# Optimization experiments

Measured on AMD Instinct MI355X. Metric: run time of the kernel, lower is better.

The kernel has to match this reference:

```python
import jax, jax.numpy as jnp
import numpy as np

N = 50000      # nodes
E = 800000     # edges
IN = 128       # in_channels
H = 64         # hidden (= edge_dim)
OUT = 64       # out_channels
BN_EPS = 1e-5


def _bn(h, gamma, beta):
    # BatchNorm1d in training mode: per-feature batch statistics
    mu = h.mean(axis=0)
    var = h.var(axis=0)
    return gamma * (h - mu) * jax.lax.rsqrt(var + BN_EPS) + beta


def _gine_layer(x, src, dst, edge_attr, We, be, W1, b1, g, bb, W2, b2):
    # edge_attr projected to node feature dim: [E, d_in]
    ea = edge_attr @ We.T + be
    # message: relu(x_j + lin(edge_attr)); x_j = x[src]
    m = jax.nn.relu(x[src] + ea)
    # scatter-add aggregate at destination nodes
    agg = jax.ops.segment_sum(m, dst, num_segments=x.shape[0])
    # (1 + eps) * x_r with eps = 0
    out = agg + x
    # MLP: Linear -> BN -> ReLU -> Linear
    h = jax.nn.relu(_bn(out @ W1.T + b1, g, bb))
    return h @ W2.T + b2


def setup_inputs() -> dict:
    key = jax.random.key(0)
    ks = jax.random.split(key, 12)

    def glorot(k, shape):
        return jax.random.normal(k, shape, jnp.float32) / np.float32(np.sqrt(shape[1]))

    return {
        "x": jax.random.normal(ks[0], (N, IN), jnp.float32),
        "edge_index": jax.random.randint(ks[1], (2, E), 0, N, jnp.int64),
        "edge_attr": jax.random.normal(ks[2], (E, H), jnp.float32),
        # layer 0
        "We0": glorot(ks[3], (IN, H)), "be0": jnp.zeros((IN,), jnp.float32),
        "W1_0": glorot(ks[4], (H, IN)), "b1_0": jnp.zeros((H,), jnp.float32),
        "g0": jnp.ones((H,), jnp.float32), "bb0": jnp.zeros((H,), jnp.float32),
        "W2_0": glorot(ks[5], (H, H)), "b2_0": jnp.zeros((H,), jnp.float32),
        # layer 1
        "We1": glorot(ks[6], (H, H)), "be1": jnp.zeros((H,), jnp.float32),
        "W1_1": glorot(ks[7], (H, H)), "b1_1": jnp.zeros((H,), jnp.float32),
        "g1": jnp.ones((H,), jnp.float32), "bb1": jnp.zeros((H,), jnp.float32),
        "W2_1": glorot(ks[8], (OUT, H)), "b2_1": jnp.zeros((OUT,), jnp.float32),
    }


def reference(x, edge_index, edge_attr,
              We0, be0, W1_0, b1_0, g0, bb0, W2_0, b2_0,
              We1, be1, W1_1, b1_1, g1, bb1, W2_1, b2_1):
    src, dst = edge_index[0], edge_index[1]
    h = _gine_layer(x, src, dst, edge_attr, We0, be0, W1_0, b1_0, g0, bb0, W2_0, b2_0)
    h = jax.nn.relu(h)  # dropout p=0.0 -> identity
    return _gine_layer(h, src, dst, edge_attr, We1, be1, W1_1, b1_1, g1, bb1, W2_1, b2_1)
```

## Files before the change

kernel.cpp:

```cpp
#include <hip/hip_runtime.h>
#include <hip/hip_bf16.h>


typedef short short8 __attribute__((ext_vector_type(8)));
typedef float f32x4 __attribute__((ext_vector_type(4)));

__device__ __forceinline__ short f2bf(float x) {
    unsigned u = __float_as_uint(x);
    unsigned r = (u + 0x7fffu + ((u >> 16) & 1u)) >> 16;
    return (short)r;
}
__device__ __forceinline__ float bf2f(unsigned short u) {
    return __uint_as_float(((unsigned)u) << 16);
}

__global__ __launch_bounds__(256) void hist_kernel(
    const int* __restrict__ ei, int* __restrict__ cnt, int E)
{
    int e = blockIdx.x * 256 + threadIdx.x;
    if (e < E) atomicAdd(&cnt[ei[E + e]], 1);
}

__global__ __launch_bounds__(1024) void scan_kernel(
    const int* __restrict__ cnt, int* __restrict__ offs,
    int* __restrict__ cursor, int N)
{
    __shared__ int wsum[16];
    __shared__ int chunk_base;
    int tid = threadIdx.x;
    int lane = tid & 63, wid = tid >> 6;
    if (tid == 0) chunk_base = 0;
    __syncthreads();
    for (int start = 0; start < N; start += 1024) {
        int i = start + tid;
        int v = (i < N) ? cnt[i] : 0;
        int s = v;
#pragma unroll
        for (int d = 1; d < 64; d <<= 1) {
            int t = __shfl_up(s, d);
            if (lane >= d) s += t;
        }
        if (lane == 63) wsum[wid] = s;
        __syncthreads();
        int wbase = 0;
        for (int w = 0; w < wid; ++w) wbase += wsum[w];
        int excl = chunk_base + wbase + s - v;
        if (i < N) { offs[i] = excl; cursor[i] = excl; }
        int tot = 0;
        for (int w = 0; w < 16; ++w) tot += wsum[w];
        __syncthreads();
        if (tid == 0) chunk_base += tot;
        __syncthreads();
    }
    if (threadIdx.x == 0) offs[N] = chunk_base;
}

__global__ __launch_bounds__(256) void scatter_kernel(
    const int* __restrict__ ei, int* __restrict__ cursor,
    int* __restrict__ inv, int E)
{
    int e = blockIdx.x * 256 + threadIdx.x;
    if (e >= E) return;
    int d = ei[E + e];
    int pos = atomicAdd(&cursor[d], 1);
    inv[e] = pos;
}

__global__ __launch_bounds__(256) void xcast_kernel(
    const float* __restrict__ x, unsigned short* __restrict__ xb, int total)
{
    for (int i = blockIdx.x * 256 + threadIdx.x; i < total; i += gridDim.x * 256)
        xb[i] = (unsigned short)f2bf(x[i]);
}

template<int DIN>
__global__ __launch_bounds__(256) void edge2_kernel(
    const unsigned short* __restrict__ xb,
    const int*    __restrict__ ei,
    const float*  __restrict__ eattr,
    const short*  __restrict__ WeB,
    const float*  __restrict__ be,
    const short*  __restrict__ W1B,
    const int*    __restrict__ inv,
    unsigned short* __restrict__ pbuf,
    int E)
{
    constexpr int S = DIN + 8;
    constexpr int KK = DIN / 32;
    __shared__ short lds[4][16][S];
    const int wave = threadIdx.x >> 6;
    const int lane = threadIdx.x & 63;
    const int ebase = (blockIdx.x * 4 + wave) * 16;
    if (ebase >= E) return;
    const int g = lane >> 4, c = lane & 15;
    short* myl = &lds[wave][0][0];

    int ce = ebase + c; if (ce >= E) ce = E - 1;
    int se_c = ei[ce];

    int sp[4];
#pragma unroll
    for (int r = 0; r < 4; ++r) {
        int e = ebase + g * 4 + r;
        sp[r] = (e < E) ? inv[e] : -1;
    }

    const float* ar = eattr + (size_t)ce * 64 + g * 8;
    f32x4 a0 = *(const f32x4*)(ar);
    f32x4 a1 = *(const f32x4*)(ar + 4);
    f32x4 a2v = *(const f32x4*)(ar + 32);
    f32x4 a3 = *(const f32x4*)(ar + 36);

    short8 xv[KK];
    const unsigned short* xr = xb + (size_t)se_c * DIN + g * 8;
#pragma unroll
    for (int kk = 0; kk < KK; ++kk)
        xv[kk] = *(const short8*)(xr + kk * 32);
    __builtin_amdgcn_sched_barrier(0);

    short8 afr0, afr1;
    afr0[0]=f2bf(a0[0]); afr0[1]=f2bf(a0[1]); afr0[2]=f2bf(a0[2]); afr0[3]=f2bf(a0[3]);
    afr0[4]=f2bf(a1[0]); afr0[5]=f2bf(a1[1]); afr0[6]=f2bf(a1[2]); afr0[7]=f2bf(a1[3]);
    afr1[0]=f2bf(a2v[0]); afr1[1]=f2bf(a2v[1]); afr1[2]=f2bf(a2v[2]); afr1[3]=f2bf(a2v[3]);
    afr1[4]=f2bf(a3[0]); afr1[5]=f2bf(a3[1]); afr1[6]=f2bf(a3[2]); afr1[7]=f2bf(a3[3]);

#pragma unroll
    for (int fc = 0; fc < DIN / 16; ++fc) {
        const short* brow = WeB + (size_t)(fc * 16 + c) * 64 + g * 8;
        short8 b0 = *(const short8*)(brow);
        short8 b1 = *(const short8*)(brow + 32);
        f32x4 acc = {0.f, 0.f, 0.f, 0.f};
        acc = __builtin_amdgcn_mfma_f32_16x16x32_bf16(afr0, b0, acc, 0, 0, 0);
        acc = __builtin_amdgcn_mfma_f32_16x16x32_bf16(afr1, b1, acc, 0, 0, 0);
        const int f = fc * 16 + c;
        const float bev = be[f];
#pragma unroll
        for (int r = 0; r < 4; ++r)
            myl[(g * 4 + r) * S + f] = f2bf(acc[r] + bev);
    }

    asm volatile("s_waitcnt lgkmcnt(0)" ::: "memory");
    __builtin_amdgcn_sched_barrier(0);

    short8 a2[KK];
#pragma unroll
    for (int kk = 0; kk < KK; ++kk) {
        short8 v = *(const short8*)(myl + c * S + kk * 32 + g * 8);
#pragma unroll
        for (int j = 0; j < 8; ++j) {
            float f = bf2f((unsigned short)v[j]) + bf2f((unsigned short)xv[kk][j]);
            a2[kk][j] = f2bf(fmaxf(f, 0.f));
        }
    }

#pragma unroll
    for (int cc = 0; cc < 4; ++cc) {
        f32x4 acc2 = {0.f, 0.f, 0.f, 0.f};
#pragma unroll
        for (int kk = 0; kk < KK; ++kk) {
            short8 b0 = *(const short8*)(W1B + (size_t)(cc * 16 + c) * DIN + kk * 32 + g * 8);
            acc2 = __builtin_amdgcn_mfma_f32_16x16x32_bf16(a2[kk], b0, acc2, 0, 0, 0);
        }
#pragma unroll
        for (int r = 0; r < 4; ++r)
            if (sp[r] >= 0)
                pbuf[(size_t)sp[r] * 64 + cc * 16 + c] = (unsigned short)f2bf(acc2[r]);
    }
}

__global__ __launch_bounds__(256) void edge1_kernel(
    const unsigned short* __restrict__ yb,
    const int*    __restrict__ ei,
    const float*  __restrict__ eattr,
    const short*  __restrict__ WeB,
    const float*  __restrict__ be,
    const int*    __restrict__ inv,
    unsigned short* __restrict__ pbuf,
    int E)
{
    constexpr int S = 72;
    __shared__ short lds[4][16][S];
    const int wave = threadIdx.x >> 6;
    const int lane = threadIdx.x & 63;
    const int ebase = (blockIdx.x * 4 + wave) * 16;
    if (ebase >= E) return;
    const int g = lane >> 4, c = lane & 15;
    short* myl = &lds[wave][0][0];

    int ce = ebase + c;
    bool cv = ce < E;
    if (!cv) ce = E - 1;
    int se_c = ei[ce];
    int sp_c = cv ? inv[ce] : -1;

    const float* ar = eattr + (size_t)ce * 64 + g * 8;
    f32x4 a0 = *(const f32x4*)(ar);
    f32x4 a1 = *(const f32x4*)(ar + 4);
    f32x4 a2v = *(const f32x4*)(ar + 32);
    f32x4 a3 = *(const f32x4*)(ar + 36);

    short8 xv0, xv1;
    {
        const unsigned short* xr = yb + (size_t)se_c * 64 + g * 8;
        xv0 = *(const short8*)(xr);
        xv1 = *(const short8*)(xr + 32);
    }
    __builtin_amdgcn_sched_barrier(0);

    short8 afr0, afr1;
    afr0[0]=f2bf(a0[0]); afr0[1]=f2bf(a0[1]); afr0[2]=f2bf(a0[2]); afr0[3]=f2bf(a0[3]);
    afr0[4]=f2bf(a1[0]); afr0[5]=f2bf(a1[1]); afr0[6]=f2bf(a1[2]); afr0[7]=f2bf(a1[3]);
    afr1[0]=f2bf(a2v[0]); afr1[1]=f2bf(a2v[1]); afr1[2]=f2bf(a2v[2]); afr1[3]=f2bf(a2v[3]);
    afr1[4]=f2bf(a3[0]); afr1[5]=f2bf(a3[1]); afr1[6]=f2bf(a3[2]); afr1[7]=f2bf(a3[3]);

#pragma unroll
    for (int fc = 0; fc < 4; ++fc) {
        const short* brow = WeB + (size_t)(fc * 16 + c) * 64 + g * 8;
        short8 b0 = *(const short8*)(brow);
        short8 b1 = *(const short8*)(brow + 32);
        f32x4 acc = {0.f, 0.f, 0.f, 0.f};
        acc = __builtin_amdgcn_mfma_f32_16x16x32_bf16(afr0, b0, acc, 0, 0, 0);
        acc = __builtin_amdgcn_mfma_f32_16x16x32_bf16(afr1, b1, acc, 0, 0, 0);
        const int f = fc * 16 + c;
        const float bev = be[f];
#pragma unroll
        for (int r = 0; r < 4; ++r)
            myl[(g * 4 + r) * S + f] = f2bf(acc[r] + bev);
    }

    asm volatile("s_waitcnt lgkmcnt(0)" ::: "memory");
    __builtin_amdgcn_sched_barrier(0);

    short8 v0 = *(const short8*)(myl + c * S + g * 8);
    short8 v1 = *(const short8*)(myl + c * S + 32 + g * 8);
    short8 out0, out1;
#pragma unroll
    for (int j = 0; j < 8; ++j) {
        float f0 = bf2f((unsigned short)v0[j]) + bf2f((unsigned short)xv0[j]);
        out0[j] = f2bf(fmaxf(f0, 0.f));
        float f1 = bf2f((unsigned short)v1[j]) + bf2f((unsigned short)xv1[j]);
        out1[j] = f2bf(fmaxf(f1, 0.f));
    }
    if (sp_c >= 0) {
        *(short8*)(pbuf + (size_t)sp_c * 64 + g * 8) = out0;
        *(short8*)(pbuf + (size_t)sp_c * 64 + 32 + g * 8) = out1;
    }
}

template<int DIN>
__global__ __launch_bounds__(256) void ngemm_kernel(
    const unsigned short* __restrict__ A,
    const short* __restrict__ W, const float* __restrict__ b,
    float* __restrict__ out, int N)
{
    constexpr int KK = DIN / 32;
    const int wave = threadIdx.x >> 6;
    const int lane = threadIdx.x & 63;
    const int nbase = (blockIdx.x * 4 + wave) * 16;
    if (nbase >= N) return;
    const int g = lane >> 4, c = lane & 15;

    int rowc = nbase + c; if (rowc >= N) rowc = N - 1;
    const unsigned short* arow = A + (size_t)rowc * DIN + g * 8;
    short8 afr[KK];
#pragma unroll
    for (int kk = 0; kk < KK; ++kk)
        afr[kk] = *(const short8*)(arow + kk * 32);

#pragma unroll
    for (int cc = 0; cc < 4; ++cc) {
        const float bev = b[cc * 16 + c];
        f32x4 acc = {bev, bev, bev, bev};
#pragma unroll
        for (int kk = 0; kk < KK; ++kk) {
            short8 bw = *(const short8*)(W + (size_t)(cc * 16 + c) * DIN + kk * 32 + g * 8);
            acc = __builtin_amdgcn_mfma_f32_16x16x32_bf16(afr[kk], bw, acc, 0, 0, 0);
        }
#pragma unroll
        for (int r = 0; r < 4; ++r) {
            int row = nbase + g * 4 + r;
            if (row < N) out[(size_t)row * 64 + cc * 16 + c] = acc[r];
        }
    }
}

__global__ __launch_bounds__(256) void ngemm_bn_kernel(
    const float* __restrict__ t, const float* __restrict__ scsh,
    const short* __restrict__ W2, const float* __restrict__ b2,
    float* __restrict__ out, unsigned short* __restrict__ outb,
    int N, int relu_out)
{
    const int wave = threadIdx.x >> 6;
    const int lane = threadIdx.x & 63;
    const int nbase = (blockIdx.x * 4 + wave) * 16;
    if (nbase >= N) return;
    const int g = lane >> 4, c = lane & 15;

    int rowc = nbase + c; if (rowc >= N) rowc = N - 1;
    const float* trow = t + (size_t)rowc * 64 + g * 8;

    short8 afr[2];
#pragma unroll
    for (int kk = 0; kk < 2; ++kk) {
        f32x4 q0 = *(const f32x4*)(trow + kk * 32);
        f32x4 q1 = *(const f32x4*)(trow + kk * 32 + 4);
        const int kbase = kk * 32 + g * 8;
        f32x4 sc0 = *(const f32x4*)(scsh + kbase);
        f32x4 sc1 = *(const f32x4*)(scsh + kbase + 4);
        f32x4 sh0 = *(const f32x4*)(scsh + 64 + kbase);
        f32x4 sh1 = *(const f32x4*)(scsh + 64 + kbase + 4);
#pragma unroll
        for (int j = 0; j < 4; ++j) {
            afr[kk][j]     = f2bf(fmaxf(q0[j] * sc0[j] + sh0[j], 0.f));
            afr[kk][j + 4] = f2bf(fmaxf(q1[j] * sc1[j] + sh1[j], 0.f));
        }
    }

#pragma unroll
    for (int cc = 0; cc < 4; ++cc) {
        const float bev = b2[cc * 16 + c];
        f32x4 acc = {bev, bev, bev, bev};
#pragma unroll
        for (int kk = 0; kk < 2; ++kk) {
            short8 bw = *(const short8*)(W2 + (size_t)(cc * 16 + c) * 64 + kk * 32 + g * 8);
            acc = __builtin_amdgcn_mfma_f32_16x16x32_bf16(afr[kk], bw, acc, 0, 0, 0);
        }
#pragma unroll
        for (int r = 0; r < 4; ++r) {
            int row = nbase + g * 4 + r;
            if (row < N) {
                float v = acc[r];
                if (relu_out) {
                    v = fmaxf(v, 0.f);
                    outb[(size_t)row * 64 + cc * 16 + c] = (unsigned short)f2bf(v);
                }
                out[(size_t)row * 64 + cc * 16 + c] = v;
            }
        }
    }
}

__global__ __launch_bounds__(256) void gather0_kernel(
    const unsigned short* __restrict__ pbuf,
    const int* __restrict__ offs,
    const float* __restrict__ xw1, float* __restrict__ t, int N)
{
    int wid = threadIdx.x >> 6, lane = threadIdx.x & 63;
    int n = blockIdx.x * 4 + wid;
    if (n >= N) return;
    float acc = xw1[(size_t)n * 64 + lane];
    int i0 = offs[n], i1 = offs[n + 1];
    const unsigned short* p = pbuf + (size_t)i0 * 64 + lane;
    int cnt = i1 - i0;
    int i = 0;
    for (; i + 3 < cnt; i += 4) {
        acc += bf2f(p[0]) + bf2f(p[64]) + bf2f(p[128]) + bf2f(p[192]);
        p += 256;
    }
    for (; i < cnt; ++i) { acc += bf2f(p[0]); p += 64; }
    t[(size_t)n * 64 + lane] = acc;
}

__global__ __launch_bounds__(256) void gathersum1_kernel(
    const unsigned short* __restrict__ pbuf,
    const int* __restrict__ offs,
    const float* __restrict__ y0, unsigned short* __restrict__ sb, int N)
{
    int wid = threadIdx.x >> 6, lane = threadIdx.x & 63;
    int n = blockIdx.x * 4 + wid;
    if (n >= N) return;
    float s = y0[(size_t)n * 64 + lane];
    int i0 = offs[n], i1 = offs[n + 1];
    const unsigned short* p = pbuf + (size_t)i0 * 64 + lane;
    int cnt = i1 - i0;
    int i = 0;
    for (; i + 3 < cnt; i += 4) {
        s += bf2f(p[0]) + bf2f(p[64]) + bf2f(p[128]) + bf2f(p[192]);
        p += 256;
    }
    for (; i < cnt; ++i) { s += bf2f(p[0]); p += 64; }
    sb[(size_t)n * 64 + lane] = (unsigned short)f2bf(s);
}

__global__ __launch_bounds__(256) void bnstats_kernel(
    const float* __restrict__ t, float* __restrict__ sums, int total)
{
    int tid = threadIdx.x;
    float s = 0.f, s2 = 0.f;
    for (int i = blockIdx.x * 256 + tid; i < total; i += gridDim.x * 256) {
        float v = t[i];
        s += v; s2 += v * v;
    }
    __shared__ float ls[256], ls2[256];
    ls[tid] = s; ls2[tid] = s2;
    __syncthreads();
    if (tid < 64) {
        s  = ls[tid]  + ls[tid + 64]  + ls[tid + 128]  + ls[tid + 192];
        s2 = ls2[tid] + ls2[tid + 64] + ls2[tid + 128] + ls2[tid + 192];
        atomicAdd(&sums[tid], s);
        atomicAdd(&sums[64 + tid], s2);
    }
}

__global__ void bnfinal_kernel(const float* __restrict__ sums,
                               const float* __restrict__ g,
                               const float* __restrict__ bb,
                               float* __restrict__ scsh, float invN)
{
    int f = threadIdx.x;
    float mean = sums[f] * invN;
    float var  = sums[64 + f] * invN - mean * mean;
    float sc = g[f] * rsqrtf(var + 1e-5f);
    scsh[f] = sc;
    scsh[64 + f] = bb[f] - mean * sc;
}

__global__ __launch_bounds__(256) void prep_kernel(
    const float* __restrict__ We0, const float* __restrict__ W1_0,
    const float* __restrict__ We1, const float* __restrict__ W1_1,
    const float* __restrict__ W2_0, const float* __restrict__ W2_1,
    short* __restrict__ WeB0, short* __restrict__ W1B0,
    short* __restrict__ WeB1, short* __restrict__ W1B1,
    short* __restrict__ W2B0, short* __restrict__ W2B1)
{
    int i = blockIdx.x * 256 + threadIdx.x;
    if (i < 128 * 64) WeB0[i] = f2bf(We0[i]);
    if (i < 64 * 128) W1B0[i] = f2bf(W1_0[i]);
    if (i < 64 * 64) {
        WeB1[i] = f2bf(We1[i]);
        W1B1[i] = f2bf(W1_1[i]);
        W2B0[i] = f2bf(W2_0[i]);
        W2B1[i] = f2bf(W2_1[i]);
    }
}

extern "C" void kernel_launch(void* const* d_in, const int* in_sizes, int n_in,
                              void* d_out, int out_size, void* d_ws, size_t ws_size,
                              hipStream_t stream)
{
    (void)n_in; (void)out_size; (void)ws_size;
    const float* x     = (const float*)d_in[0];
    const int*   ei    = (const int*)d_in[1];
    const float* eattr = (const float*)d_in[2];
    const float* We0   = (const float*)d_in[3];
    const float* be0   = (const float*)d_in[4];
    const float* W1_0  = (const float*)d_in[5];
    const float* b1_0  = (const float*)d_in[6];
    const float* g0    = (const float*)d_in[7];
    const float* bb0   = (const float*)d_in[8];
    const float* W2_0  = (const float*)d_in[9];
    const float* b2_0  = (const float*)d_in[10];
    const float* We1   = (const float*)d_in[11];
    const float* be1   = (const float*)d_in[12];
    const float* W1_1  = (const float*)d_in[13];
    const float* b1_1  = (const float*)d_in[14];
    const float* g1    = (const float*)d_in[15];
    const float* bb1   = (const float*)d_in[16];
    const float* W2_1  = (const float*)d_in[17];
    const float* b2_1  = (const float*)d_in[18];
    float* out = (float*)d_out;

    const int N = in_sizes[0] / 128;
    const int E = in_sizes[2] / 64;

    char* ws = (char*)d_ws;
    size_t o = 0;
    auto alloc = [&](size_t bytes) { char* p = ws + o; o = (o + bytes + 255) & ~(size_t)255; return p; };
    unsigned short* pbuf = (unsigned short*)alloc((size_t)E * 64 * 2);
    float* tbuf   = (float*)alloc((size_t)N * 64 * 4);
    float* y0     = (float*)alloc((size_t)N * 64 * 4);
    unsigned short* xb = (unsigned short*)alloc((size_t)N * 128 * 2);
    unsigned short* yb = (unsigned short*)alloc((size_t)N * 64 * 2);
    short* WeB0   = (short*)alloc(128 * 64 * 2);
    short* W1B0   = (short*)alloc(64 * 128 * 2);
    short* WeB1   = (short*)alloc(64 * 64 * 2);
    short* W1B1   = (short*)alloc(64 * 64 * 2);
    short* W2B0   = (short*)alloc(64 * 64 * 2);
    short* W2B1   = (short*)alloc(64 * 64 * 2);
    float* stats  = (float*)alloc(512 * 4);
    int*   cnt    = (int*)alloc((size_t)N * 4);
    int*   offs   = (int*)alloc((size_t)(N + 1) * 4);
    int*   inv    = (int*)alloc((size_t)E * 4);
    float* sum0  = stats;
    float* scsh0 = stats + 128;
    float* sum1  = stats + 256;
    float* scsh1 = stats + 384;
    float* xw1f  = y0;
    unsigned short* sb = yb;

    hipMemsetAsync(stats, 0, 512 * 4, stream);
    hipMemsetAsync(cnt, 0, (size_t)N * 4, stream);
    prep_kernel<<<64, 256, 0, stream>>>(We0, W1_0, We1, W1_1, W2_0, W2_1,
                                        WeB0, W1B0, WeB1, W1B1, W2B0, W2B1);
    xcast_kernel<<<2048, 256, 0, stream>>>(x, xb, N * 128);

    const int eb256 = (E + 255) / 256;

    hist_kernel<<<eb256, 256, 0, stream>>>(ei, cnt, E);
    scan_kernel<<<1, 1024, 0, stream>>>(cnt, offs, cnt, N);
    scatter_kernel<<<eb256, 256, 0, stream>>>(ei, cnt, inv, E);

    const int edge_blocks = (E + 63) / 64;
    const int n4_blocks   = (N + 3) / 4;
    const int nt_blocks   = ((N + 15) / 16 + 3) / 4;

    edge2_kernel<128><<<edge_blocks, 256, 0, stream>>>(
        xb, ei, eattr, WeB0, be0, W1B0, inv, pbuf, E);
    ngemm_kernel<128><<<nt_blocks, 256, 0, stream>>>(xb, W1B0, b1_0, xw1f, N);
    gather0_kernel<<<n4_blocks, 256, 0, stream>>>(pbuf, offs, xw1f, tbuf, N);
    bnstats_kernel<<<256, 256, 0, stream>>>(tbuf, sum0, N * 64);
    bnfinal_kernel<<<1, 64, 0, stream>>>(sum0, g0, bb0, scsh0, 1.0f / N);
    ngemm_bn_kernel<<<nt_blocks, 256, 0, stream>>>(
        tbuf, scsh0, W2B0, b2_0, y0, yb, N, 1);

    edge1_kernel<<<edge_blocks, 256, 0, stream>>>(
        yb, ei, eattr, WeB1, be1, inv, pbuf, E);
    gathersum1_kernel<<<n4_blocks, 256, 0, stream>>>(pbuf, offs, y0, sb, N);
    ngemm_kernel<64><<<nt_blocks, 256, 0, stream>>>(sb, W1B1, b1_1, tbuf, N);
    bnstats_kernel<<<256, 256, 0, stream>>>(tbuf, sum1, N * 64);
    bnfinal_kernel<<<1, 64, 0, stream>>>(sum1, g1, bb1, scsh1, 1.0f / N);
    ngemm_bn_kernel<<<nt_blocks, 256, 0, stream>>>(
        tbuf, scsh1, W2B1, b2_1, out, yb, N, 0);
}
```

Before: 615.3 us.

## Move layer-0 W1 projection from per-edge to per-node after aggregation

The layer-0 edge kernel no longer multiplies each message by W1. It writes the full 128-wide relu(x_j+ea) message, and the gather sums these with x before a node-level GEMM applies W1. This cuts the per-edge matmul work by exploiting linearity of the aggregation, and removes the LDS round trip through a lane-to-feature remapping. In exchange, the per-edge message buffer doubles in width, which raises write and gather memory traffic.

```diff
diff --git a/kernel.cpp b/kernel.cpp
--- a/kernel.cpp
+++ b/kernel.cpp
@@ -2,8 +2,10 @@
 #include <hip/hip_bf16.h>
 
 
+typedef short bhalf4 __attribute__((ext_vector_type(4)));
 typedef short short8 __attribute__((ext_vector_type(8)));
 typedef float f32x4 __attribute__((ext_vector_type(4)));
+typedef float f32x2 __attribute__((ext_vector_type(2)));
 
 __device__ __forceinline__ short f2bf(float x) {
     unsigned u = __float_as_uint(x);
@@ -73,292 +75,102 @@
         xb[i] = (unsigned short)f2bf(x[i]);
 }
 
-template<int DIN>
-__global__ __launch_bounds__(256) void edge2_kernel(
+template<int DF>
+__global__ __launch_bounds__(256) void edgem_kernel(
     const unsigned short* __restrict__ xb,
     const int*    __restrict__ ei,
     const float*  __restrict__ eattr,
-    const short*  __restrict__ WeB,
+    const short*  __restrict__ WB,
     const float*  __restrict__ be,
-    const short*  __restrict__ W1B,
     const int*    __restrict__ inv,
     unsigned short* __restrict__ pbuf,
     int E)
 {
-    constexpr int S = DIN + 8;
-    constexpr int KK = DIN / 32;
-    __shared__ short lds[4][16][S];
+    constexpr int FC = DF / 16;
     const int wave = threadIdx.x >> 6;
     const int lane = threadIdx.x & 63;
     const int ebase = (blockIdx.x * 4 + wave) * 16;
     if (ebase >= E) return;
     const int g = lane >> 4, c = lane & 15;
-    short* myl = &lds[wave][0][0];
-
-    int ce = ebase + c; if (ce >= E) ce = E - 1;
-    int se_c = ei[ce];
-
-    int sp[4];
-#pragma unroll
-    for (int r = 0; r < 4; ++r) {
-        int e = ebase + g * 4 + r;
-        sp[r] = (e < E) ? inv[e] : -1;
-    }
-
-    const float* ar = eattr + (size_t)ce * 64 + g * 8;
+
+    int ce = ebase + c;
+    bool cv = ce < E;
+    int ces = cv ? ce : (E - 1);
+    int se = ei[ces];
+    int sp = cv ? inv[ces] : -1;
+
+    const float* ar = eattr + (size_t)ces * 64 + g * 8;
     f32x4 a0 = *(const f32x4*)(ar);
     f32x4 a1 = *(const f32x4*)(ar + 4);
-    f32x4 a2v = *(const f32x4*)(ar + 32);
+    f32x4 a2 = *(const f32x4*)(ar + 32);
     f32x4 a3 = *(const f32x4*)(ar + 36);
 
-    short8 xv[KK];
-    const unsigned short* xr = xb + (size_t)se_c * DIN + g * 8;
-#pragma unroll
-    for (int kk = 0; kk < KK; ++kk)
-        xv[kk] = *(const short8*)(xr + kk * 32);
+    bhalf4 xv[FC];
+    const unsigned short* xr = xb + (size_t)se * DF + g * 4;
+#pragma unroll
+    for (int fc = 0; fc < FC; ++fc)
+        xv[fc] = *(const bhalf4*)(xr + fc * 16);
     __builtin_amdgcn_sched_barrier(0);
 
-    short8 afr0, afr1;
-    afr0[0]=f2bf(a0[0]); afr0[1]=f2bf(a0[1]); afr0[2]=f2bf(a0[2]); afr0[3]=f2bf(a0[3]);
-    afr0[4]=f2bf(a1[0]); afr0[5]=f2bf(a1[1]); afr0[6]=f2bf(a1[2]); afr0[7]=f2bf(a1[3]);
-    afr1[0]=f2bf(a2v[0]); afr1[1]=f2bf(a2v[1]); afr1[2]=f2bf(a2v[2]); afr1[3]=f2bf(a2v[3]);
-    afr1[4]=f2bf(a3[0]); afr1[5]=f2bf(a3[1]); afr1[6]=f2bf(a3[2]); afr1[7]=f2bf(a3[3]);
-
-#pragma unroll
-    for (int fc = 0; fc < DIN / 16; ++fc) {
-        const short* brow = WeB + (size_t)(fc * 16 + c) * 64 + g * 8;
-        short8 b0 = *(const short8*)(brow);
-        short8 b1 = *(const short8*)(brow + 32);
+    short8 bfr0, bfr1;
+    bfr0[0]=f2bf(a0[0]); bfr0[1]=f2bf(a0[1]); bfr0[2]=f2bf(a0[2]); bfr0[3]=f2bf(a0[3]);
+    bfr0[4]=f2bf(a1[0]); bfr0[5]=f2bf(a1[1]); bfr0[6]=f2bf(a1[2]); bfr0[7]=f2bf(a1[3]);
+    bfr1[0]=f2bf(a2[0]); bfr1[1]=f2bf(a2[1]); bfr1[2]=f2bf(a2[2]); bfr1[3]=f2bf(a2[3]);
+    bfr1[4]=f2bf(a3[0]); bfr1[5]=f2bf(a3[1]); bfr1[6]=f2bf(a3[2]); bfr1[7]=f2bf(a3[3]);
+
+#pragma unroll
+    for (int fc = 0; fc < FC; ++fc) {
+        const short* aw = WB + (size_t)(fc * 16 + c) * 64 + g * 8;
+        short8 aw0 = *(const short8*)(aw);
+        short8 aw1 = *(const short8*)(aw + 32);
         f32x4 acc = {0.f, 0.f, 0.f, 0.f};
-        acc = __builtin_amdgcn_mfma_f32_16x16x32_bf16(afr0, b0, acc, 0, 0, 0);
-        acc = __builtin_amdgcn_mfma_f32_16x16x32_bf16(afr1, b1, acc, 0, 0, 0);
-        const int f = fc * 16 + c;
-        const float bev = be[f];
-#pragma unroll
-        for (int r = 0; r < 4; ++r)
-            myl[(g * 4 + r) * S + f] = f2bf(acc[r] + bev);
-    }
-
-    asm volatile("s_waitcnt lgkmcnt(0)" ::: "memory");
-    __builtin_amdgcn_sched_barrier(0);
-
-    short8 a2[KK];
-#pragma unroll
-    for (int kk = 0; kk < KK; ++kk) {
-        short8 v = *(const short8*)(myl + c * S + kk * 32 + g * 8);
-#pragma unroll
-        for (int j = 0; j < 8; ++j) {
-            float f = bf2f((unsigned short)v[j]) + bf2f((unsigned short)xv[kk][j]);
-            a2[kk][j] = f2bf(fmaxf(f, 0.f));
-        }
-    }
-
-#pragma unroll
-    for (int cc = 0; cc < 4; ++cc) {
-        f32x4 acc2 = {0.f, 0.f, 0.f, 0.f};
-#pragma unroll
-        for (int kk = 0; kk < KK; ++kk) {
-            short8 b0 = *(const short8*)(W1B + (size_t)(cc * 16 + c) * DIN + kk * 32 + g * 8);
-            acc2 = __builtin_amdgcn_mfma_f32_16x16x32_bf16(a2[kk], b0, acc2, 0, 0, 0);
-        }
-#pragma unroll
-        for (int r = 0; r < 4; ++r)
-            if (sp[r] >= 0)
-                pbuf[(size_t)sp[r] * 64 + cc * 16 + c] = (unsigned short)f2bf(acc2[r]);
-    }
-}
-
-__global__ __launch_bounds__(256) void edge1_kernel(
-    const unsigned short* __restrict__ yb,
-    const int*    __restrict__ ei,
-    const float*  __restrict__ eattr,
-    const short*  __restrict__ WeB,
-    const float*  __restrict__ be,
-    const int*    __restrict__ inv,
-    unsigned short* __restrict__ pbuf,
-    int E)
-{
-    constexpr int S = 72;
-    __shared__ short lds[4][16][S];
-    const int wave = threadIdx.x >> 6;
-    const int lane = threadIdx.x & 63;
-    const int ebase = (blockIdx.x * 4 + wave) * 16;
-    if (ebase >= E) return;
-    const int g = lane >> 4, c = lane & 15;
-    short* myl = &lds[wave][0][0];
-
-    int ce = ebase + c;
-    bool cv = ce < E;
-    if (!cv) ce = E - 1;
-    int se_c = ei[ce];
-    int sp_c = cv ? inv[ce] : -1;
-
-    const float* ar = eattr + (size_t)ce * 64 + g * 8;
-    f32x4 a0 = *(const f32x4*)(ar);
-    f32x4 a1 = *(const f32x4*)(ar + 4);
-    f32x4 a2v = *(const f32x4*)(ar + 32);
-    f32x4 a3 = *(const f32x4*)(ar + 36);
-
-    short8 xv0, xv1;
-    {
-        const unsigned short* xr = yb + (size_t)se_c * 64 + g * 8;
-        xv0 = *(const short8*)(xr);
-        xv1 = *(const short8*)(xr + 32);
-    }
-    __builtin_amdgcn_sched_barrier(0);
-
-    short8 afr0, afr1;
-    afr0[0]=f2bf(a0[0]); afr0[1]=f2bf(a0[1]); afr0[2]=f2bf(a0[2]); afr0[3]=f2bf(a0[3]);
-    afr0[4]=f2bf(a1[0]); afr0[5]=f2bf(a1[1]); afr0[6]=f2bf(a1[2]); afr0[7]=f2bf(a1[3]);
-    afr1[0]=f2bf(a2v[0]); afr1[1]=f2bf(a2v[1]); afr1[2]=f2bf(a2v[2]); afr1[3]=f2bf(a2v[3]);
-    afr1[4]=f2bf(a3[0]); afr1[5]=f2bf(a3[1]); afr1[6]=f2bf(a3[2]); afr1[7]=f2bf(a3[3]);
-
-#pragma unroll
-    for (int fc = 0; fc < 4; ++fc) {
-        const short* brow = WeB + (size_t)(fc * 16 + c) * 64 + g * 8;
-        short8 b0 = *(const short8*)(brow);
-        short8 b1 = *(const short8*)(brow + 32);
-        f32x4 acc = {0.f, 0.f, 0.f, 0.f};
-        acc = __builtin_amdgcn_mfma_f32_16x16x32_bf16(afr0, b0, acc, 0, 0, 0);
-        acc = __builtin_amdgcn_mfma_f32_16x16x32_bf16(afr1, b1, acc, 0, 0, 0);
-        const int f = fc * 16 + c;
-        const float bev = be[f];
-#pragma unroll
-        for (int r = 0; r < 4; ++r)
-            myl[(g * 4 + r) * S + f] = f2bf(acc[r] + bev);
-    }
-
-    asm volatile("s_waitcnt lgkmcnt(0)" ::: "memory");
-    __builtin_amdgcn_sched_barrier(0);
-
-    short8 v0 = *(const short8*)(myl + c * S + g * 8);
-    short8 v1 = *(const short8*)(myl + c * S + 32 + g * 8);
-    short8 out0, out1;
-#pragma unroll
-    for (int j = 0; j < 8; ++j) {
-        float f0 = bf2f((unsigned short)v0[j]) + bf2f((unsigned short)xv0[j]);
-        out0[j] = f2bf(fmaxf(f0, 0.f));
-        float f1 = bf2f((unsigned short)v1[j]) + bf2f((unsigned short)xv1[j]);
-        out1[j] = f2bf(fmaxf(f1, 0.f));
-    }
-    if (sp_c >= 0) {
-        *(short8*)(pbuf + (size_t)sp_c * 64 + g * 8) = out0;
-        *(short8*)(pbuf + (size_t)sp_c * 64 + 32 + g * 8) = out1;
-    }
-}
-
-template<int DIN>
-__global__ __launch_bounds__(256) void ngemm_kernel(
-    const unsigned short* __restrict__ A,
-    const short* __restrict__ W, const float* __restrict__ b,
-    float* __restrict__ out, int N)
-{
-    constexpr int KK = DIN / 32;
-    const int wave = threadIdx.x >> 6;
-    const int lane = threadIdx.x & 63;
-    const int nbase = (blockIdx.x * 4 + wave) * 16;
-    if (nbase >= N) return;
-    const int g = lane >> 4, c = lane & 15;
-
-    int rowc = nbase + c; if (rowc >= N) rowc = N - 1;
-    const unsigned short* arow = A + (size_t)rowc * DIN + g * 8;
-    short8 afr[KK];
-#pragma unroll
-    for (int kk = 0; kk < KK; ++kk)
-        afr[kk] = *(const short8*)(arow + kk * 32);
-
-#pragma unroll
-    for (int cc = 0; cc < 4; ++cc) {
-        const float bev = b[cc * 16 + c];
-        f32x4 acc = {bev, bev, bev, bev};
-#pragma unroll
-        for (int kk = 0; kk < KK; ++kk) {
-            short8 bw = *(const short8*)(W + (size_t)(cc * 16 + c) * DIN + kk * 32 + g * 8);
-            acc = __builtin_amdgcn_mfma_f32_16x16x32_bf16(afr[kk], bw, acc, 0, 0, 0);
-        }
+        acc = __builtin_amdgcn_mfma_f32_16x16x32_bf16(aw0, bfr0, acc, 0, 0, 0);
+        acc = __builtin_amdgcn_mfma_f32_16x16x32_bf16(aw1, bfr1, acc, 0, 0, 0);
+
+        f32x4 bev = *(const f32x4*)(be + fc * 16 + g * 4);
+        bhalf4 outp;
 #pragma unroll
         for (int r = 0; r < 4; ++r) {
-            int row = nbase + g * 4 + r;
-            if (row < N) out[(size_t)row * 64 + cc * 16 + c] = acc[r];
-        }
-    }
-}
-
-__global__ __launch_bounds__(256) void ngemm_bn_kernel(
-    const float* __restrict__ t, const float* __restrict__ scsh,
-    const short* __restrict__ W2, const float* __restrict__ b2,
-    float* __restrict__ out, unsigned short* __restrict__ outb,
-    int N, int relu_out)
-{
-    const int wave = threadIdx.x >> 6;
-    const int lane = threadIdx.x & 63;
-    const int nbase = (blockIdx.x * 4 + wave) * 16;
-    if (nbase >= N) return;
-    const int g = lane >> 4, c = lane & 15;
-
-    int rowc = nbase + c; if (rowc >= N) rowc = N - 1;
-    const float* trow = t + (size_t)rowc * 64 + g * 8;
-
-    short8 afr[2];
-#pragma unroll
-    for (int kk = 0; kk < 2; ++kk) {
-        f32x4 q0 = *(const f32x4*)(trow + kk * 32);
-        f32x4 q1 = *(const f32x4*)(trow + kk * 32 + 4);
-        const int kbase = kk * 32 + g * 8;
-        f32x4 sc0 = *(const f32x4*)(scsh + kbase);
-        f32x4 sc1 = *(const f32x4*)(scsh + kbase + 4);
-        f32x4 sh0 = *(const f32x4*)(scsh + 64 + kbase);
-        f32x4 sh1 = *(const f32x4*)(scsh + 64 + kbase + 4);
-#pragma unroll
-        for (int j = 0; j < 4; ++j) {
-            afr[kk][j]     = f2bf(fmaxf(q0[j] * sc0[j] + sh0[j], 0.f));
-            afr[kk][j + 4] = f2bf(fmaxf(q1[j] * sc1[j] + sh1[j], 0.f));
-        }
-    }
-
-#pragma unroll
-    for (int cc = 0; cc < 4; ++cc) {
-        const float bev = b2[cc * 16 + c];
-        f32x4 acc = {bev, bev, bev, bev};
-#pragma unroll
-        for (int kk = 0; kk < 2; ++kk) {
-            short8 bw = *(const short8*)(W2 + (size_t)(cc * 16 + c) * 64 + kk * 32 + g * 8);
-            acc = __builtin_amdgcn_mfma_f32_16x16x32_bf16(afr[kk], bw, acc, 0, 0, 0);
-        }
-#pragma unroll
-        for (int r = 0; r < 4; ++r) {
-            int row = nbase + g * 4 + r;
-            if (row < N) {
-                float v = acc[r];
-                if (relu_out) {
-                    v = fmaxf(v, 0.f);
-                    outb[(size_t)row * 64 + cc * 16 + c] = (unsigned short)f2bf(v);
-                }
-                out[(size_t)row * 64 + cc * 16 + c] = v;
-            }
-        }
-    }
-}
-
-__global__ __launch_bounds__(256) void gather0_kernel(
+            float v = acc[r] + bev[r] + bf2f((unsigned short)xv[fc][r]);
+            outp[r] = f2bf(fmaxf(v, 0.f));
+        }
+        if (sp >= 0)
+            *(bhalf4*)(pbuf + (size_t)sp * DF + fc * 16 + g * 4) = outp;
+    }
+}
+
+__global__ __launch_bounds__(256) void gathersum0_kernel(
     const unsigned short* __restrict__ pbuf,
     const int* __restrict__ offs,
-    const float* __restrict__ xw1, float* __restrict__ t, int N)
+    const float* __restrict__ x,
+    unsigned short* __restrict__ sb, int N)
 {
     int wid = threadIdx.x >> 6, lane = threadIdx.x & 63;
     int n = blockIdx.x * 4 + wid;
     if (n >= N) return;
-    float acc = xw1[(size_t)n * 64 + lane];
+    f32x2 xx = *(const f32x2*)(x + (size_t)n * 128 + 2 * lane);
+    float s0 = xx[0], s1 = xx[1];
     int i0 = offs[n], i1 = offs[n + 1];
-    const unsigned short* p = pbuf + (size_t)i0 * 64 + lane;
+    const unsigned int* p = (const unsigned int*)(pbuf + (size_t)i0 * 128) + lane;
     int cnt = i1 - i0;
     int i = 0;
     for (; i + 3 < cnt; i += 4) {
-        acc += bf2f(p[0]) + bf2f(p[64]) + bf2f(p[128]) + bf2f(p[192]);
+        unsigned int v0 = p[0], v1 = p[64], v2 = p[128], v3 = p[192];
+        s0 += bf2f((unsigned short)v0) + bf2f((unsigned short)v1)
+            + bf2f((unsigned short)v2) + bf2f((unsigned short)v3);
+        s1 += bf2f((unsigned short)(v0 >> 16)) + bf2f((unsigned short)(v1 >> 16))
+            + bf2f((unsigned short)(v2 >> 16)) + bf2f((unsigned short)(v3 >> 16));
         p += 256;
     }
-    for (; i < cnt; ++i) { acc += bf2f(p[0]); p += 64; }
-    t[(size_t)n * 64 + lane] = acc;
+    for (; i < cnt; ++i) {
+        unsigned int v = p[0];
+        s0 += bf2f((unsigned short)v);
+        s1 += bf2f((unsigned short)(v >> 16));
+        p += 64;
+    }
+    unsigned int packed = (unsigned int)(unsigned short)f2bf(s0)
+                        | ((unsigned int)(unsigned short)f2bf(s1) << 16);
+    *(unsigned int*)(sb + (size_t)n * 128 + 2 * lane) = packed;
 }
 
 __global__ __launch_bounds__(256) void gathersum1_kernel(
@@ -380,6 +192,99 @@
     }
     for (; i < cnt; ++i) { s += bf2f(p[0]); p += 64; }
     sb[(size_t)n * 64 + lane] = (unsigned short)f2bf(s);
+}
+
+template<int DIN>
+__global__ __launch_bounds__(256) void ngemm_kernel(
+    const unsigned short* __restrict__ A,
+    const short* __restrict__ W, const float* __restrict__ b,
+    float* __restrict__ out, int N)
+{
+    constexpr int KK = DIN / 32;
+    const int wave = threadIdx.x >> 6;
+    const int lane = threadIdx.x & 63;
+    const int nbase = (blockIdx.x * 4 + wave) * 16;
+    if (nbase >= N) return;
+    const int g = lane >> 4, c = lane & 15;
+
+    int rowc = nbase + c; if (rowc >= N) rowc = N - 1;
+    const unsigned short* arow = A + (size_t)rowc * DIN + g * 8;
+    short8 afr[KK];
+#pragma unroll
+    for (int kk = 0; kk < KK; ++kk)
+        afr[kk] = *(const short8*)(arow + kk * 32);
+
+#pragma unroll
+    for (int cc = 0; cc < 4; ++cc) {
+        const float bev = b[cc * 16 + c];
+        f32x4 acc = {bev, bev, bev, bev};
+#pragma unroll
+        for (int kk = 0; kk < KK; ++kk) {
+            short8 bw = *(const short8*)(W + (size_t)(cc * 16 + c) * DIN + kk * 32 + g * 8);
+            acc = __builtin_amdgcn_mfma_f32_16x16x32_bf16(afr[kk], bw, acc, 0, 0, 0);
+        }
+#pragma unroll
+        for (int r = 0; r < 4; ++r) {
+            int row = nbase + g * 4 + r;
+            if (row < N) out[(size_t)row * 64 + cc * 16 + c] = acc[r];
+        }
+    }
+}
+
+__global__ __launch_bounds__(256) void ngemm_bn_kernel(
+    const float* __restrict__ t, const float* __restrict__ scsh,
+    const short* __restrict__ W2, const float* __restrict__ b2,
+    float* __restrict__ out, unsigned short* __restrict__ outb,
+    int N, int relu_out)
+{
+    const int wave = threadIdx.x >> 6;
+    const int lane = threadIdx.x & 63;
+    const int nbase = (blockIdx.x * 4 + wave) * 16;
+    if (nbase >= N) return;
+    const int g = lane >> 4, c = lane & 15;
+
+    int rowc = nbase + c; if (rowc >= N) rowc = N - 1;
+    const float* trow = t + (size_t)rowc * 64 + g * 8;
+
+    short8 afr[2];
+#pragma unroll
+    for (int kk = 0; kk < 2; ++kk) {
+        f32x4 q0 = *(const f32x4*)(trow + kk * 32);
+        f32x4 q1 = *(const f32x4*)(trow + kk * 32 + 4);
+        const int kbase = kk * 32 + g * 8;
+        f32x4 sc0 = *(const f32x4*)(scsh + kbase);
+        f32x4 sc1 = *(const f32x4*)(scsh + kbase + 4);
+        f32x4 sh0 = *(const f32x4*)(scsh + 64 + kbase);
+        f32x4 sh1 = *(const f32x4*)(scsh + 64 + kbase + 4);
+#pragma unroll
+        for (int j = 0; j < 4; ++j) {
+            afr[kk][j]     = f2bf(fmaxf(q0[j] * sc0[j] + sh0[j], 0.f));
+            afr[kk][j + 4] = f2bf(fmaxf(q1[j] * sc1[j] + sh1[j], 0.f));
+        }
+    }
+
+#pragma unroll
+    for (int cc = 0; cc < 4; ++cc) {
+        const float bev = b2[cc * 16 + c];
+        f32x4 acc = {bev, bev, bev, bev};
+#pragma unroll
+        for (int kk = 0; kk < 2; ++kk) {
+            short8 bw = *(const short8*)(W2 + (size_t)(cc * 16 + c) * 64 + kk * 32 + g * 8);
+            acc = __builtin_amdgcn_mfma_f32_16x16x32_bf16(afr[kk], bw, acc, 0, 0, 0);
+        }
+#pragma unroll
+        for (int r = 0; r < 4; ++r) {
+            int row = nbase + g * 4 + r;
+            if (row < N) {
+                float v = acc[r];
+                if (relu_out) {
+                    v = fmaxf(v, 0.f);
+                    outb[(size_t)row * 64 + cc * 16 + c] = (unsigned short)f2bf(v);
+                }
+                out[(size_t)row * 64 + cc * 16 + c] = v;
+            }
+        }
+    }
 }
 
 __global__ __launch_bounds__(256) void bnstats_kernel(
@@ -466,7 +371,7 @@
     char* ws = (char*)d_ws;
     size_t o = 0;
     auto alloc = [&](size_t bytes) { char* p = ws + o; o = (o + bytes + 255) & ~(size_t)255; return p; };
-    unsigned short* pbuf = (unsigned short*)alloc((size_t)E * 64 * 2);
+    unsigned short* pbuf = (unsigned short*)alloc((size_t)E * 128 * 2);
     float* tbuf   = (float*)alloc((size_t)N * 64 * 4);
     float* y0     = (float*)alloc((size_t)N * 64 * 4);
     unsigned short* xb = (unsigned short*)alloc((size_t)N * 128 * 2);
@@ -485,11 +390,11 @@
     float* scsh0 = stats + 128;
     float* sum1  = stats + 256;
     float* scsh1 = stats + 384;
-    float* xw1f  = y0;
-    unsigned short* sb = yb;
-
-    hipMemsetAsync(stats, 0, 512 * 4, stream);
-    hipMemsetAsync(cnt, 0, (size_t)N * 4, stream);
+    unsigned short* sb0 = xb;
+    unsigned short* sb1 = yb;
+
+    (void)hipMemsetAsync(stats, 0, 512 * 4, stream);
+    (void)hipMemsetAsync(cnt, 0, (size_t)N * 4, stream);
     prep_kernel<<<64, 256, 0, stream>>>(We0, W1_0, We1, W1_1, W2_0, W2_1,
                                         WeB0, W1B0, WeB1, W1B1, W2B0, W2B1);
     xcast_kernel<<<2048, 256, 0, stream>>>(x, xb, N * 128);
@@ -500,23 +405,23 @@
     scan_kernel<<<1, 1024, 0, stream>>>(cnt, offs, cnt, N);
     scatter_kernel<<<eb256, 256, 0, stream>>>(ei, cnt, inv, E);
 
-    const int edge_blocks = (E + 63) / 64;
+    const int edge_blocks = ((E + 15) / 16 + 3) / 4;
     const int n4_blocks   = (N + 3) / 4;
     const int nt_blocks   = ((N + 15) / 16 + 3) / 4;
 
-    edge2_kernel<128><<<edge_blocks, 256, 0, stream>>>(
-        xb, ei, eattr, WeB0, be0, W1B0, inv, pbuf, E);
-    ngemm_kernel<128><<<nt_blocks, 256, 0, stream>>>(xb, W1B0, b1_0, xw1f, N);
-    gather0_kernel<<<n4_blocks, 256, 0, stream>>>(pbuf, offs, xw1f, tbuf, N);
+    edgem_kernel<128><<<edge_blocks, 256, 0, stream>>>(
+        xb, ei, eattr, WeB0, be0, inv, pbuf, E);
+    gathersum0_kernel<<<n4_blocks, 256, 0, stream>>>(pbuf, offs, x, sb0, N);
+    ngemm_kernel<128><<<nt_blocks, 256, 0, stream>>>(sb0, W1B0, b1_0, tbuf, N);
     bnstats_kernel<<<256, 256, 0, stream>>>(tbuf, sum0, N * 64);
     bnfinal_kernel<<<1, 64, 0, stream>>>(sum0, g0, bb0, scsh0, 1.0f / N);
     ngemm_bn_kernel<<<nt_blocks, 256, 0, stream>>>(
         tbuf, scsh0, W2B0, b2_0, y0, yb, N, 1);
 
-    edge1_kernel<<<edge_blocks, 256, 0, stream>>>(
+    edgem_kernel<64><<<edge_blocks, 256, 0, stream>>>(
         yb, ei, eattr, WeB1, be1, inv, pbuf, E);
-    gathersum1_kernel<<<n4_blocks, 256, 0, stream>>>(pbuf, offs, y0, sb, N);
-    ngemm_kernel<64><<<nt_blocks, 256, 0, stream>>>(sb, W1B1, b1_1, tbuf, N);
+    gathersum1_kernel<<<n4_blocks, 256, 0, stream>>>(pbuf, offs, y0, sb1, N);
+    ngemm_kernel<64><<<nt_blocks, 256, 0, stream>>>(sb1, W1B1, b1_1, tbuf, N);
     bnstats_kernel<<<256, 256, 0, stream>>>(tbuf, sum1, N * 64);
     bnfinal_kernel<<<1, 64, 0, stream>>>(sum1, g1, bb1, scsh1, 1.0f / N);
     ngemm_bn_kernel<<<nt_blocks, 256, 0, stream>>>(
```

New measurement: 647.0 us. +5.1%, slower.
